# Kernel optimization log

Measured on AMD Instinct MI355X. Metric: run time of the kernel, lower is better.

Reference implementation:

```python
import jax, jax.numpy as jnp
import numpy as np

NUM_HEADS = 16
DIM_IN = 1024
DIM_HIDDEN = 1024
DIM_OUT = 1024
DIM_HEAD = DIM_HIDDEN // NUM_HEADS


def setup_inputs() -> dict:
    key = jax.random.key(0)
    kx, kw1, kw2 = jax.random.split(key, 3)
    B, L = 4, 2048
    x = jax.random.normal(kx, (B, L, DIM_IN), dtype=jnp.float32)
    # xavier_uniform for qkv weight: shape (3*dim_hidden, dim_in) in torch; keep torch layout
    limit_qkv = float(np.sqrt(6.0 / (DIM_IN + 3 * DIM_HIDDEN)))
    W_qkv = jax.random.uniform(kw1, (3 * DIM_HIDDEN, DIM_IN), dtype=jnp.float32,
                               minval=-limit_qkv, maxval=limit_qkv)
    b_qkv = jnp.zeros((3 * DIM_HIDDEN,), dtype=jnp.float32)
    limit_out = float(np.sqrt(6.0 / (DIM_HIDDEN + DIM_OUT)))
    W_out = jax.random.uniform(kw2, (DIM_OUT, DIM_HIDDEN), dtype=jnp.float32,
                               minval=-limit_out, maxval=limit_out)
    b_out = jnp.zeros((DIM_OUT,), dtype=jnp.float32)
    return {"x": x, "W_qkv": W_qkv, "b_qkv": b_qkv, "W_out": W_out, "b_out": b_out}


def reference(x, W_qkv, b_qkv, W_out, b_out):
    B, L, _ = x.shape
    # fused qkv projection: (B, L, 3*dim_hidden)
    qkv = jnp.einsum('bld,ed->ble', x, W_qkv) + b_qkv
    # faithful reshape: (B, L, H, 3*dim_head) then permute to (B, H, L, 3*dim_head)
    qkv = qkv.reshape(B, L, NUM_HEADS, 3 * DIM_HEAD).transpose(0, 2, 1, 3)
    q, k, v = jnp.split(qkv, 3, axis=-1)  # each (B, H, L, dim_head)
    scores = jnp.einsum('bhqd,bhkd->bhqk', q, k) / jnp.sqrt(jnp.float32(DIM_HEAD))
    attn = jax.nn.softmax(scores, axis=-1)
    logits = jnp.einsum('bhqk,bhkd->bhqd', attn, v)
    logits = logits.transpose(0, 2, 1, 3).reshape(B, L, DIM_HIDDEN)
    out = jnp.einsum('blh,oh->blo', logits, W_out) + b_out
    return out
```

## Files before the change

### kernel.cpp

```cpp
#include <hip/hip_runtime.h>
#include <hip/hip_bf16.h>


typedef __attribute__((ext_vector_type(8))) short short8;
typedef __attribute__((ext_vector_type(4))) float f32x4;
typedef __attribute__((ext_vector_type(4))) unsigned int uint32x4;

#define DEV static __device__ __forceinline__

DEV unsigned short f2bf(float f) {
  __hip_bfloat16 h = __float2bfloat16(f);
  return __builtin_bit_cast(unsigned short, h);
}

DEV unsigned int cvt_pk_bf16(float lo, float hi) {
  unsigned int r;
  asm("v_cvt_pk_bf16_f32 %0, %1, %2" : "=v"(r) : "v"(lo), "v"(hi));
  return r;
}

#define PLS32(a, b) asm("v_permlane32_swap_b32 %0, %1" : "+v"(a), "+v"(b))
#define PLS16(a, b) asm("v_permlane16_swap_b32 %0, %1" : "+v"(a), "+v"(b))

DEV void gld_lds16(void* lds, const void* g) {
  __builtin_amdgcn_global_load_lds(
      (const __attribute__((address_space(1))) unsigned int*)g,
      (__attribute__((address_space(3))) unsigned int*)lds, 16, 0, 0);
}

DEV f32x4 mfma16(short8 a, short8 b, f32x4 c) {
  return __builtin_amdgcn_mfma_f32_16x16x32_bf16(a, b, c, 0, 0, 0);
}

__global__ __launch_bounds__(256) void k_cvt(const float* __restrict__ s,
                                             unsigned short* __restrict__ d, int n4) {
  int i = blockIdx.x * 256 + threadIdx.x;
  if (i >= n4) return;
  float4 v = ((const float4*)s)[i];
  ushort4 o;
  o.x = f2bf(v.x); o.y = f2bf(v.y); o.z = f2bf(v.z); o.w = f2bf(v.w);
  ((ushort4*)d)[i] = o;
}

__global__ __launch_bounds__(256) void k_gemm_qkv(
    const unsigned short* __restrict__ A, const unsigned short* __restrict__ Bw,
    const float* __restrict__ bias,
    unsigned short* __restrict__ Qg, unsigned short* __restrict__ Kg,
    unsigned short* __restrict__ Vg) {
  __shared__ unsigned short As[128 * 32];
  __shared__ unsigned short Bs[128 * 32];
  const int tid = threadIdx.x, lane = tid & 63, w = tid >> 6;
  const int m0 = blockIdx.y * 128, n0 = blockIdx.x * 128;
  const int wr = w >> 1, wc = w & 1;
  const int col = lane & 15, kg = lane >> 4;
  f32x4 acc[4][4] = {};
  const int K = 1024;
  for (int k0 = 0; k0 < K; k0 += 32) {
#pragma unroll
    for (int j = 0; j < 2; ++j) {
      const int rr = (j * 4 + w) * 16;
      const int row = rr + (lane >> 2);
      const int cb = (lane & 3) * 16;
      gld_lds16((char*)As + rr * 64, (const char*)(A + (size_t)(m0 + row) * K + k0) + cb);
      gld_lds16((char*)Bs + rr * 64, (const char*)(Bw + (size_t)(n0 + row) * K + k0) + cb);
    }
    __syncthreads();
    short8 af[4], bfr[4];
#pragma unroll
    for (int mi = 0; mi < 4; mi++)
      af[mi] = *(const short8*)(As + (wr * 64 + mi * 16 + col) * 32 + kg * 8);
#pragma unroll
    for (int ni = 0; ni < 4; ni++)
      bfr[ni] = *(const short8*)(Bs + (wc * 64 + ni * 16 + col) * 32 + kg * 8);
#pragma unroll
    for (int mi = 0; mi < 4; mi++)
#pragma unroll
      for (int ni = 0; ni < 4; ni++)
        acc[mi][ni] = mfma16(af[mi], bfr[ni], acc[mi][ni]);
    __syncthreads();
  }
  const float QSCALE = 0.1803368801111204f;
#pragma unroll
  for (int mi = 0; mi < 4; mi++) {
#pragma unroll
    for (int ni = 0; ni < 4; ni++) {
#pragma unroll
      for (int r = 0; r < 4; r++) {
        const int grow = m0 + wr * 64 + mi * 16 + kg * 4 + r;
        const int gcol = n0 + wc * 64 + ni * 16 + col;
        float v = acc[mi][ni][r] + bias[gcol];
        const int h = gcol / 192, c = gcol % 192;
        const int bh = (grow >> 11) * 16 + h;
        const size_t base = ((size_t)bh * 2048 + (grow & 2047)) * 64;
        if (c < 64) Qg[base + c] = f2bf(v * QSCALE);
        else if (c < 128) Kg[base + (c - 64)] = f2bf(v);
        else Vg[base + (c - 128)] = f2bf(v);
      }
    }
  }
}

__global__ __launch_bounds__(256) void k_transpose(const unsigned short* __restrict__ V,
                                                   unsigned short* __restrict__ Vt) {
  __shared__ unsigned short t[64][72];
  const int tid = threadIdx.x;
  const int bh = blockIdx.y, l0 = blockIdx.x * 64;
#pragma unroll
  for (int i = 0; i < 2; i++) {
    const int slot = i * 256 + tid;
    const int r = slot >> 3, c0 = (slot & 7) * 8;
    short8 v = *(const short8*)(V + ((size_t)bh * 2048 + l0 + r) * 64 + c0);
#pragma unroll
    for (int j = 0; j < 8; j++) t[c0 + j][r] = (unsigned short)v[j];
  }
  __syncthreads();
#pragma unroll
  for (int i = 0; i < 2; i++) {
    const int slot = i * 256 + tid;
    const int d = slot >> 3, x0 = (slot & 7) * 8;
    short8 o;
#pragma unroll
    for (int j = 0; j < 8; j++) o[j] = (short)t[d][x0 + j];
    *(short8*)(Vt + ((size_t)bh * 64 + d) * 2048 + l0 + x0) = o;
  }
}

__global__ __launch_bounds__(256, 3) void k_attn(const unsigned short* __restrict__ Qg,
                                                 const unsigned short* __restrict__ Kg,
                                                 const unsigned short* __restrict__ Vtg,
                                                 unsigned short* __restrict__ Lg) {
  __shared__ unsigned short Ks[2][64 * 64];
  __shared__ unsigned short Vs[2][64 * 64];
  const int tid = threadIdx.x, lane = tid & 63, w = tid >> 6;

  const int id = blockIdx.x + (blockIdx.y << 4);
  const int xcd = id & 7, slot = id >> 3;
  const int bh = ((slot >> 4) << 3) + xcd;
  const int q0 = (slot & 15) * 128 + w * 32;
  const int col = lane & 15, kg = lane >> 4;

  short8 qa[2][2];
#pragma unroll
  for (int sub = 0; sub < 2; sub++) {
    const unsigned short* qbase = Qg + ((size_t)bh * 2048 + q0 + sub * 16 + col) * 64 + kg * 8;
    qa[sub][0] = *(const short8*)(qbase);
    qa[sub][1] = *(const short8*)(qbase + 32);
  }

  f32x4 accO[2][4] = {};
  float lp[2] = {0.f, 0.f};

  const int st_row8 = lane >> 3;
  const int st_cb = (lane & 7) * 16;

  auto STAGE = [&](int buf, int kt) {
#pragma unroll
    for (int j = 0; j < 2; ++j) {
      const int rr = (j * 4 + w) * 8;
      const int row = rr + st_row8;
      const int sc = st_cb ^ ((row & 7) << 4);
      gld_lds16((char*)&Ks[buf][0] + rr * 128,
                (const char*)(Kg + ((size_t)bh * 2048 + kt * 64 + row) * 64) + sc);
      gld_lds16((char*)&Vs[buf][0] + rr * 128,
                (const char*)(Vtg + ((size_t)bh * 64 + row) * 2048 + (size_t)kt * 64) + sc);
    }
  };

  STAGE(0, 0);

  const int xr = (col & 7) << 4;
  const int x0 = (kg * 16) ^ xr;
  const int x1 = (64 + kg * 16) ^ xr;

  for (int kt = 0; kt < 32; ++kt) {
    const int cur = kt & 1;
    __syncthreads();
    if (kt < 31) STAGE(cur ^ 1, kt + 1);

    const char* KsB = (const char*)&Ks[cur][0];
    const char* VsB = (const char*)&Vs[cur][0];

    short8 kf[4][2];
#pragma unroll
    for (int n = 0; n < 4; n++) {
      const char* kb = KsB + (n * 16 + col) * 128;
      kf[n][0] = *(const short8*)(kb + x0);
      kf[n][1] = *(const short8*)(kb + x1);
    }

    short8 pa[2][2];
#pragma unroll
    for (int sub = 0; sub < 2; sub++) {
      f32x4 s[4];
      __builtin_amdgcn_s_setprio(1);
#pragma unroll
      for (int n = 0; n < 4; n++) {
        s[n] = f32x4{0.f, 0.f, 0.f, 0.f};
        s[n] = mfma16(kf[n][0], qa[sub][0], s[n]);
        s[n] = mfma16(kf[n][1], qa[sub][1], s[n]);
      }
      __builtin_amdgcn_s_setprio(0);
      unsigned int wv[4][2];
#pragma unroll
      for (int n = 0; n < 4; n++) {
        const float p0 = __builtin_amdgcn_exp2f(s[n][0]);
        const float p1 = __builtin_amdgcn_exp2f(s[n][1]);
        const float p2 = __builtin_amdgcn_exp2f(s[n][2]);
        const float p3 = __builtin_amdgcn_exp2f(s[n][3]);
        lp[sub] += (p0 + p1) + (p2 + p3);
        wv[n][0] = cvt_pk_bf16(p0, p1);
        wv[n][1] = cvt_pk_bf16(p2, p3);
      }
      PLS32(wv[0][0], wv[1][0]);
      PLS32(wv[0][1], wv[1][1]);
      PLS16(wv[0][0], wv[1][0]);
      PLS16(wv[0][1], wv[1][1]);
      PLS32(wv[2][0], wv[3][0]);
      PLS32(wv[2][1], wv[3][1]);
      PLS16(wv[2][0], wv[3][0]);
      PLS16(wv[2][1], wv[3][1]);
      uint32x4 u0 = {wv[0][0], wv[0][1], wv[1][0], wv[1][1]};
      uint32x4 u1 = {wv[2][0], wv[2][1], wv[3][0], wv[3][1]};
      pa[sub][0] = __builtin_bit_cast(short8, u0);
      pa[sub][1] = __builtin_bit_cast(short8, u1);
    }

    __builtin_amdgcn_s_setprio(1);
#pragma unroll
    for (int df = 0; df < 4; df++) {
      const char* vb = VsB + (df * 16 + col) * 128;
      const short8 vf0 = *(const short8*)(vb + x0);
      const short8 vf1 = *(const short8*)(vb + x1);
      accO[0][df] = mfma16(pa[0][0], vf0, accO[0][df]);
      accO[0][df] = mfma16(pa[0][1], vf1, accO[0][df]);
      accO[1][df] = mfma16(pa[1][0], vf0, accO[1][df]);
      accO[1][df] = mfma16(pa[1][1], vf1, accO[1][df]);
    }
    __builtin_amdgcn_s_setprio(0);
  }

  const int b = bh >> 4, h = bh & 15;
#pragma unroll
  for (int sub = 0; sub < 2; sub++) {
    float t = lp[sub];
    t += __shfl_xor(t, 16);
    t += __shfl_xor(t, 32);
#pragma unroll
    for (int r = 0; r < 4; r++) {
      const float rs = __shfl(t, kg * 4 + r);
      const float inv = 1.0f / rs;
      const int grow = q0 + sub * 16 + kg * 4 + r;
      unsigned short* orow = Lg + ((size_t)b * 2048 + grow) * 1024 + h * 64;
#pragma unroll
      for (int df = 0; df < 4; df++) orow[df * 16 + col] = f2bf(accO[sub][df][r] * inv);
    }
  }
}

__global__ __launch_bounds__(256) void k_gemm_out(
    const unsigned short* __restrict__ A, const unsigned short* __restrict__ Bw,
    const float* __restrict__ bias, float* __restrict__ C) {
  __shared__ unsigned short As[128 * 32];
  __shared__ unsigned short Bs[128 * 32];
  const int tid = threadIdx.x, lane = tid & 63, w = tid >> 6;
  const int m0 = blockIdx.y * 128, n0 = blockIdx.x * 128;
  const int wr = w >> 1, wc = w & 1;
  const int col = lane & 15, kg = lane >> 4;
  f32x4 acc[4][4] = {};
  const int K = 1024;
  for (int k0 = 0; k0 < K; k0 += 32) {
#pragma unroll
    for (int j = 0; j < 2; ++j) {
      const int rr = (j * 4 + w) * 16;
      const int row = rr + (lane >> 2);
      const int cb = (lane & 3) * 16;
      gld_lds16((char*)As + rr * 64, (const char*)(A + (size_t)(m0 + row) * K + k0) + cb);
      gld_lds16((char*)Bs + rr * 64, (const char*)(Bw + (size_t)(n0 + row) * K + k0) + cb);
    }
    __syncthreads();
    short8 af[4], bfr[4];
#pragma unroll
    for (int mi = 0; mi < 4; mi++)
      af[mi] = *(const short8*)(As + (wr * 64 + mi * 16 + col) * 32 + kg * 8);
#pragma unroll
    for (int ni = 0; ni < 4; ni++)
      bfr[ni] = *(const short8*)(Bs + (wc * 64 + ni * 16 + col) * 32 + kg * 8);
#pragma unroll
    for (int mi = 0; mi < 4; mi++)
#pragma unroll
      for (int ni = 0; ni < 4; ni++)
        acc[mi][ni] = mfma16(af[mi], bfr[ni], acc[mi][ni]);
    __syncthreads();
  }
#pragma unroll
  for (int mi = 0; mi < 4; mi++) {
#pragma unroll
    for (int ni = 0; ni < 4; ni++) {
#pragma unroll
      for (int r = 0; r < 4; r++) {
        const int grow = m0 + wr * 64 + mi * 16 + kg * 4 + r;
        const int gcol = n0 + wc * 64 + ni * 16 + col;
        C[(size_t)grow * 1024 + gcol] = acc[mi][ni][r] + bias[gcol];
      }
    }
  }
}

extern "C" void kernel_launch(void* const* d_in, const int* in_sizes, int n_in,
                              void* d_out, int out_size, void* d_ws, size_t ws_size,
                              hipStream_t stream) {
  (void)in_sizes; (void)n_in; (void)out_size; (void)ws_size;
  const float* x    = (const float*)d_in[0];
  const float* Wqkv = (const float*)d_in[1];
  const float* bqkv = (const float*)d_in[2];
  const float* Wout = (const float*)d_in[3];
  const float* bout = (const float*)d_in[4];
  float* out = (float*)d_out;

  char* ws = (char*)d_ws;
  unsigned short* Xb  = (unsigned short*)(ws);
  unsigned short* Wqb = (unsigned short*)(ws + 16777216);
  unsigned short* Wob = (unsigned short*)(ws + 23068672);
  unsigned short* Qg  = (unsigned short*)(ws + 25165824);
  unsigned short* Kg  = (unsigned short*)(ws + 41943040);
  unsigned short* Vg  = (unsigned short*)(ws + 58720256);
  unsigned short* Vt  = (unsigned short*)(ws + 75497472);
  unsigned short* Lg  = Xb;

  k_cvt<<<8192, 256, 0, stream>>>(x, Xb, 2097152);
  k_cvt<<<3072, 256, 0, stream>>>(Wqkv, Wqb, 786432);
  k_cvt<<<1024, 256, 0, stream>>>(Wout, Wob, 262144);
  k_gemm_qkv<<<dim3(24, 64), 256, 0, stream>>>(Xb, Wqb, bqkv, Qg, Kg, Vg);
  k_transpose<<<dim3(32, 64), 256, 0, stream>>>(Vg, Vt);
  k_attn<<<dim3(16, 64), 256, 0, stream>>>(Qg, Kg, Vt, Lg);
  k_gemm_out<<<dim3(8, 64), 256, 0, stream>>>(Lg, Wob, bout, out);
}
```

Measured before the change: 218.5 us.

## Double GEMM K-tile to 64 with XOR-swizzled LDS and merge conversion kernels

Both projection GEMMs now stage 64-wide K slices per iteration instead of 32. The LDS layout is XOR-swizzled so the 128-byte rows don't bank-conflict on fragment reads. This halves the number of barrier pairs per GEMM and adds more MFMA work per sync, at the cost of doubled shared memory per block. The three fp32-to-bf16 conversion launches are also fused into one kernel that dispatches on the index range, removing two launches.

```diff
diff --git a/kernel.cpp b/kernel.cpp
--- a/kernel.cpp
+++ b/kernel.cpp
@@ -32,10 +32,22 @@
   return __builtin_amdgcn_mfma_f32_16x16x32_bf16(a, b, c, 0, 0, 0);
 }
 
-__global__ __launch_bounds__(256) void k_cvt(const float* __restrict__ s,
-                                             unsigned short* __restrict__ d, int n4) {
+__global__ __launch_bounds__(256) void k_cvt3(const float* __restrict__ x,
+                                              const float* __restrict__ wq,
+                                              const float* __restrict__ wo,
+                                              unsigned short* __restrict__ dx,
+                                              unsigned short* __restrict__ dwq,
+                                              unsigned short* __restrict__ dwo) {
   int i = blockIdx.x * 256 + threadIdx.x;
-  if (i >= n4) return;
+  const float* s;
+  unsigned short* d;
+  if (i < 2097152) {
+    s = x; d = dx;
+  } else if (i < 2883584) {
+    i -= 2097152; s = wq; d = dwq;
+  } else {
+    i -= 2883584; s = wo; d = dwo;
+  }
   float4 v = ((const float4*)s)[i];
   ushort4 o;
   o.x = f2bf(v.x); o.y = f2bf(v.y); o.z = f2bf(v.z); o.w = f2bf(v.w);
@@ -47,36 +59,47 @@
     const float* __restrict__ bias,
     unsigned short* __restrict__ Qg, unsigned short* __restrict__ Kg,
     unsigned short* __restrict__ Vg) {
-  __shared__ unsigned short As[128 * 32];
-  __shared__ unsigned short Bs[128 * 32];
+  __shared__ unsigned short As[128 * 64];
+  __shared__ unsigned short Bs[128 * 64];
   const int tid = threadIdx.x, lane = tid & 63, w = tid >> 6;
   const int m0 = blockIdx.y * 128, n0 = blockIdx.x * 128;
   const int wr = w >> 1, wc = w & 1;
   const int col = lane & 15, kg = lane >> 4;
   f32x4 acc[4][4] = {};
   const int K = 1024;
-  for (int k0 = 0; k0 < K; k0 += 32) {
-#pragma unroll
-    for (int j = 0; j < 2; ++j) {
-      const int rr = (j * 4 + w) * 16;
-      const int row = rr + (lane >> 2);
-      const int cb = (lane & 3) * 16;
-      gld_lds16((char*)As + rr * 64, (const char*)(A + (size_t)(m0 + row) * K + k0) + cb);
-      gld_lds16((char*)Bs + rr * 64, (const char*)(Bw + (size_t)(n0 + row) * K + k0) + cb);
-    }
-    __syncthreads();
-    short8 af[4], bfr[4];
-#pragma unroll
-    for (int mi = 0; mi < 4; mi++)
-      af[mi] = *(const short8*)(As + (wr * 64 + mi * 16 + col) * 32 + kg * 8);
-#pragma unroll
-    for (int ni = 0; ni < 4; ni++)
-      bfr[ni] = *(const short8*)(Bs + (wc * 64 + ni * 16 + col) * 32 + kg * 8);
-#pragma unroll
-    for (int mi = 0; mi < 4; mi++)
-#pragma unroll
-      for (int ni = 0; ni < 4; ni++)
-        acc[mi][ni] = mfma16(af[mi], bfr[ni], acc[mi][ni]);
+  const int st_row = lane >> 3;
+  const int st_cb = (lane & 7) * 16;
+  const int xr = (col & 7) << 4;
+  const int x0 = (kg * 16) ^ xr;
+  const int x1 = (64 + kg * 16) ^ xr;
+  for (int k0 = 0; k0 < K; k0 += 64) {
+#pragma unroll
+    for (int j = 0; j < 4; ++j) {
+      const int rr = (j * 4 + w) * 8;
+      const int row = rr + st_row;
+      const int sc = st_cb ^ ((row & 7) << 4);
+      gld_lds16((char*)As + rr * 128, (const char*)(A + (size_t)(m0 + row) * K + k0) + sc);
+      gld_lds16((char*)Bs + rr * 128, (const char*)(Bw + (size_t)(n0 + row) * K + k0) + sc);
+    }
+    __syncthreads();
+    short8 bfr[4][2];
+#pragma unroll
+    for (int ni = 0; ni < 4; ni++) {
+      const char* bb = (const char*)Bs + (wc * 64 + ni * 16 + col) * 128;
+      bfr[ni][0] = *(const short8*)(bb + x0);
+      bfr[ni][1] = *(const short8*)(bb + x1);
+    }
+#pragma unroll
+    for (int mi = 0; mi < 4; mi++) {
+      const char* ab = (const char*)As + (wr * 64 + mi * 16 + col) * 128;
+      const short8 af0 = *(const short8*)(ab + x0);
+      const short8 af1 = *(const short8*)(ab + x1);
+#pragma unroll
+      for (int ni = 0; ni < 4; ni++) {
+        acc[mi][ni] = mfma16(af0, bfr[ni][0], acc[mi][ni]);
+        acc[mi][ni] = mfma16(af1, bfr[ni][1], acc[mi][ni]);
+      }
+    }
     __syncthreads();
   }
   const float QSCALE = 0.1803368801111204f;
@@ -260,36 +283,47 @@
 __global__ __launch_bounds__(256) void k_gemm_out(
     const unsigned short* __restrict__ A, const unsigned short* __restrict__ Bw,
     const float* __restrict__ bias, float* __restrict__ C) {
-  __shared__ unsigned short As[128 * 32];
-  __shared__ unsigned short Bs[128 * 32];
+  __shared__ unsigned short As[128 * 64];
+  __shared__ unsigned short Bs[128 * 64];
   const int tid = threadIdx.x, lane = tid & 63, w = tid >> 6;
   const int m0 = blockIdx.y * 128, n0 = blockIdx.x * 128;
   const int wr = w >> 1, wc = w & 1;
   const int col = lane & 15, kg = lane >> 4;
   f32x4 acc[4][4] = {};
   const int K = 1024;
-  for (int k0 = 0; k0 < K; k0 += 32) {
-#pragma unroll
-    for (int j = 0; j < 2; ++j) {
-      const int rr = (j * 4 + w) * 16;
-      const int row = rr + (lane >> 2);
-      const int cb = (lane & 3) * 16;
-      gld_lds16((char*)As + rr * 64, (const char*)(A + (size_t)(m0 + row) * K + k0) + cb);
-      gld_lds16((char*)Bs + rr * 64, (const char*)(Bw + (size_t)(n0 + row) * K + k0) + cb);
-    }
-    __syncthreads();
-    short8 af[4], bfr[4];
-#pragma unroll
-    for (int mi = 0; mi < 4; mi++)
-      af[mi] = *(const short8*)(As + (wr * 64 + mi * 16 + col) * 32 + kg * 8);
-#pragma unroll
-    for (int ni = 0; ni < 4; ni++)
-      bfr[ni] = *(const short8*)(Bs + (wc * 64 + ni * 16 + col) * 32 + kg * 8);
-#pragma unroll
-    for (int mi = 0; mi < 4; mi++)
-#pragma unroll
-      for (int ni = 0; ni < 4; ni++)
-        acc[mi][ni] = mfma16(af[mi], bfr[ni], acc[mi][ni]);
+  const int st_row = lane >> 3;
+  const int st_cb = (lane & 7) * 16;
+  const int xr = (col & 7) << 4;
+  const int x0 = (kg * 16) ^ xr;
+  const int x1 = (64 + kg * 16) ^ xr;
+  for (int k0 = 0; k0 < K; k0 += 64) {
+#pragma unroll
+    for (int j = 0; j < 4; ++j) {
+      const int rr = (j * 4 + w) * 8;
+      const int row = rr + st_row;
+      const int sc = st_cb ^ ((row & 7) << 4);
+      gld_lds16((char*)As + rr * 128, (const char*)(A + (size_t)(m0 + row) * K + k0) + sc);
+      gld_lds16((char*)Bs + rr * 128, (const char*)(Bw + (size_t)(n0 + row) * K + k0) + sc);
+    }
+    __syncthreads();
+    short8 bfr[4][2];
+#pragma unroll
+    for (int ni = 0; ni < 4; ni++) {
+      const char* bb = (const char*)Bs + (wc * 64 + ni * 16 + col) * 128;
+      bfr[ni][0] = *(const short8*)(bb + x0);
+      bfr[ni][1] = *(const short8*)(bb + x1);
+    }
+#pragma unroll
+    for (int mi = 0; mi < 4; mi++) {
+      const char* ab = (const char*)As + (wr * 64 + mi * 16 + col) * 128;
+      const short8 af0 = *(const short8*)(ab + x0);
+      const short8 af1 = *(const short8*)(ab + x1);
+#pragma unroll
+      for (int ni = 0; ni < 4; ni++) {
+        acc[mi][ni] = mfma16(af0, bfr[ni][0], acc[mi][ni]);
+        acc[mi][ni] = mfma16(af1, bfr[ni][1], acc[mi][ni]);
+      }
+    }
     __syncthreads();
   }
 #pragma unroll
@@ -327,9 +361,7 @@
   unsigned short* Vt  = (unsigned short*)(ws + 75497472);
   unsigned short* Lg  = Xb;
 
-  k_cvt<<<8192, 256, 0, stream>>>(x, Xb, 2097152);
-  k_cvt<<<3072, 256, 0, stream>>>(Wqkv, Wqb, 786432);
-  k_cvt<<<1024, 256, 0, stream>>>(Wout, Wob, 262144);
+  k_cvt3<<<12288, 256, 0, stream>>>(x, Wqkv, Wout, Xb, Wqb, Wob);
   k_gemm_qkv<<<dim3(24, 64), 256, 0, stream>>>(Xb, Wqb, bqkv, Qg, Kg, Vg);
   k_transpose<<<dim3(32, 64), 256, 0, stream>>>(Vg, Vt);
   k_attn<<<dim3(16, 64), 256, 0, stream>>>(Qg, Kg, Vt, Lg);
```

Measured after the change: 205.3 us. 6.0% less time.
